# Optimization experiments

Hardware: AMD Instinct MI355X
Metric: run time of the kernel (lower is better)

The kernel has to match this reference:

```python
import jax, jax.numpy as jnp
import numpy as np

N_USER, N_ENTITY, N_RELATION = 100000, 2000000, 64
BATCH, N_NEIGHBOR, DIM = 65536, 8, 16
L2_WEIGHT = 1e-4


def setup_inputs() -> dict:
    key = jax.random.key(0)
    ks = jax.random.split(key, 10)
    inp = {
        # parameters: torch.rand(..)*2-1 -> uniform(-1,1)
        "user_emb": jax.random.uniform(ks[0], (N_USER, DIM), jnp.float32, -1.0, 1.0),
        "entity_emb": jax.random.uniform(ks[1], (N_ENTITY, DIM), jnp.float32, -1.0, 1.0),
        "relation_emb": jax.random.uniform(ks[2], (N_RELATION, DIM), jnp.float32, -1.0, 1.0),
        "agg_W": jax.random.normal(ks[3], (DIM, DIM), jnp.float32) * (1.0 / np.sqrt(DIM)),
        "agg_b": jnp.zeros((DIM,), jnp.float32),
        "labels": jnp.round(jax.random.uniform(ks[4], (BATCH,), jnp.float32)),
        "user_indices": jax.random.randint(ks[5], (BATCH,), 0, N_USER, jnp.int32),
        "item_indices": jax.random.randint(ks[6], (BATCH,), 0, N_ENTITY, jnp.int32),
        "adj_entity": jax.random.randint(ks[7], (N_ENTITY, N_NEIGHBOR), 0, N_ENTITY, jnp.int32),
        "adj_relation": jax.random.randint(ks[8], (N_ENTITY, N_NEIGHBOR), 0, N_RELATION, jnp.int32),
    }
    return inp


def reference(user_emb, entity_emb, relation_emb, agg_W, agg_b, labels,
              user_indices, item_indices, adj_entity, adj_relation):
    # --- gathers (1-hop, n_iter=1) ---
    u = user_emb[user_indices]                      # [B, D]
    self_vec = entity_emb[item_indices]             # [B, D]
    nbr_e = adj_entity[item_indices]                # [B, K]
    nbr_r = adj_relation[item_indices]              # [B, K]
    nbr_vecs = entity_emb[nbr_e]                    # [B, K, D]
    rel_vecs = relation_emb[nbr_r]                  # [B, K, D]

    # --- SumAggregator: user-relation attention over neighbors ---
    scores = jnp.mean(u[:, None, :] * rel_vecs, axis=-1)     # [B, K]
    attn = jax.nn.softmax(scores, axis=-1)                   # [B, K]
    nbr_agg = jnp.einsum('bk,bkd->bd', attn, nbr_vecs)       # [B, D]

    # Linear(dim,dim) + tanh (act on last hop)
    item_emb = jnp.tanh((self_vec + nbr_agg) @ agg_W.T + agg_b)  # [B, D]

    # --- score + BCE loss + L2 ---
    logits = jnp.sum(u * item_emb, axis=1)                   # [B]
    # -y*log(sigmoid(x)) - (1-y)*log(1-sigmoid(x)), stable form
    base_loss = jnp.mean(-labels * jax.nn.log_sigmoid(logits)
                         - (1.0 - labels) * jax.nn.log_sigmoid(-logits))
    l2 = 0.5 * (jnp.sum(user_emb ** 2) + jnp.sum(entity_emb ** 2)
                + jnp.sum(relation_emb ** 2))
    return base_loss + L2_WEIGHT * l2
```

## Files before the change

### kernel.cpp

```cpp
#include <hip/hip_runtime.h>
#include <math.h>

#define BATCH     65536
#define NNBR      8
#define DIM       16
#define HALF_L2W  5.0e-5f

#define BLOCK     256
#define GRID      2048
#define N_SBLK    1024
#define STH       (N_SBLK * BLOCK)
#define ROWS_PB   64

#define N_E4      8000000
#define N_U4      400000
#define N_R4      256

#define E_ITERS   (N_E4 / STH)
#define E_TAIL    (N_E4 - E_ITERS * STH)
#define U_TAIL    (N_U4 - STH)

__device__ __forceinline__ float sq4(float4 v) {
    return v.x * v.x + v.y * v.y + v.z * v.z + v.w * v.w;
}

__global__ void __launch_bounds__(BLOCK, 4)
fused_kernel(const float4* __restrict__ ue4,
             const float4* __restrict__ ee4,
             const float4* __restrict__ re4,
             const float*  __restrict__ W,
             const float4* __restrict__ b4,
             const float*  __restrict__ labels,
             const int*    __restrict__ uidx,
             const int*    __restrict__ iidx,
             const int4*   __restrict__ adjE4,
             const int4*   __restrict__ adjR4,
             float* __restrict__ ws) {
    float l2 = 0.0f, bce = 0.0f;

    const int role = blockIdx.x & 1;
    const int rid  = blockIdx.x >> 1;

    if (role == 0) {
        const int tid = rid * BLOCK + threadIdx.x;
        const float4* p = ee4 + tid;
        #pragma unroll
        for (int k = 0; k < E_ITERS; ++k) l2 += sq4(p[k * STH]);
        if (tid < E_TAIL) l2 += sq4(p[E_ITERS * STH]);
        l2 += sq4(ue4[tid]);
        if (tid < U_TAIL) l2 += sq4(ue4[tid + STH]);
        if (tid < N_R4)   l2 += sq4(re4[tid]);
    } else {
        __shared__ float sWT[DIM * DIM];
        __shared__ float4 sb4[DIM / 4];
        if (threadIdx.x < DIM * DIM)
            sWT[threadIdx.x] = W[(threadIdx.x & 15) * DIM + (threadIdx.x >> 4)];
        if (threadIdx.x < DIM / 4) sb4[threadIdx.x] = b4[threadIdx.x];
        __syncthreads();

        const int lane4 = threadIdx.x & 3;
        const int rgrp  = threadIdx.x >> 2;
        const int row   = rid * ROWS_PB + rgrp;

        const int ui = uidx[row];
        const int it = iidx[row];
        const float4 u4  = ue4[ui * 4 + lane4];
        const float4 sv4 = ee4[it * 4 + lane4];
        const int4 a0 = adjE4[it * 2], a1 = adjE4[it * 2 + 1];
        const int4 r0 = adjR4[it * 2], r1 = adjR4[it * 2 + 1];

        const int ne[NNBR] = {a0.x, a0.y, a0.z, a0.w, a1.x, a1.y, a1.z, a1.w};
        const int nr[NNBR] = {r0.x, r0.y, r0.z, r0.w, r1.x, r1.y, r1.z, r1.w};

        float4 nv[NNBR];
        float sc[NNBR];
        #pragma unroll
        for (int k = 0; k < NNBR; ++k) {
            const float4 rv = re4[nr[k] * 4 + lane4];
            nv[k] = ee4[ne[k] * 4 + lane4];
            float s = u4.x * rv.x + u4.y * rv.y + u4.z * rv.z + u4.w * rv.w;
            s += __shfl_xor(s, 1, 4);
            s += __shfl_xor(s, 2, 4);
            sc[k] = s * (1.0f / 16.0f);
        }

        float m = sc[0];
        #pragma unroll
        for (int k = 1; k < NNBR; ++k) m = fmaxf(m, sc[k]);
        float e[NNBR], den = 0.0f;
        #pragma unroll
        for (int k = 0; k < NNBR; ++k) { e[k] = __expf(sc[k] - m); den += e[k]; }
        const float inv = 1.0f / den;

        float4 agg = make_float4(0.f, 0.f, 0.f, 0.f);
        #pragma unroll
        for (int k = 0; k < NNBR; ++k) {
            agg.x += e[k] * nv[k].x; agg.y += e[k] * nv[k].y;
            agg.z += e[k] * nv[k].z; agg.w += e[k] * nv[k].w;
        }

        float4 x4;
        x4.x = sv4.x + agg.x * inv; x4.y = sv4.y + agg.y * inv;
        x4.z = sv4.z + agg.z * inv; x4.w = sv4.w + agg.w * inv;

        float xall[DIM];
        #pragma unroll
        for (int src = 0; src < 4; ++src) {
            xall[4 * src + 0] = __shfl(x4.x, src, 4);
            xall[4 * src + 1] = __shfl(x4.y, src, 4);
            xall[4 * src + 2] = __shfl(x4.z, src, 4);
            xall[4 * src + 3] = __shfl(x4.w, src, 4);
        }

        const float4* sWT4 = (const float4*)sWT;
        float4 acc = sb4[lane4];
        #pragma unroll
        for (int j = 0; j < DIM; ++j) {
            const float4 wv = sWT4[j * 4 + lane4];
            acc.x += xall[j] * wv.x; acc.y += xall[j] * wv.y;
            acc.z += xall[j] * wv.z; acc.w += xall[j] * wv.w;
        }
        float4 item;
        item.x = tanhf(acc.x); item.y = tanhf(acc.y);
        item.z = tanhf(acc.z); item.w = tanhf(acc.w);

        float lg = u4.x * item.x + u4.y * item.y + u4.z * item.z + u4.w * item.w;
        lg += __shfl_xor(lg, 1, 4);
        lg += __shfl_xor(lg, 2, 4);

        if (lane4 == 0) {
            const float y = labels[row];
            bce = fmaxf(lg, 0.0f) - lg * y + log1pf(__expf(-fabsf(lg)));
        }
    }

    #pragma unroll
    for (int o = 32; o > 0; o >>= 1) {
        bce += __shfl_down(bce, o);
        l2  += __shfl_down(l2, o);
    }
    __shared__ float sred[8];
    const int wid = threadIdx.x >> 6;
    if ((threadIdx.x & 63) == 0) { sred[wid] = l2; sred[4 + wid] = bce; }
    __syncthreads();
    if (threadIdx.x == 0) {
        ws[2 * blockIdx.x]     = sred[0] + sred[1] + sred[2] + sred[3];
        ws[2 * blockIdx.x + 1] = sred[4] + sred[5] + sred[6] + sred[7];
    }
}

__global__ void __launch_bounds__(256)
finalize_kernel(const float* __restrict__ ws, float* __restrict__ out) {
    float l2 = 0.0f, bce = 0.0f;
    #pragma unroll
    for (int k = 0; k < GRID / 256; ++k) {
        const int i = threadIdx.x + k * 256;
        l2  += ws[2 * i];
        bce += ws[2 * i + 1];
    }
    #pragma unroll
    for (int o = 32; o > 0; o >>= 1) {
        l2  += __shfl_down(l2, o);
        bce += __shfl_down(bce, o);
    }
    __shared__ float sred[8];
    const int wid = threadIdx.x >> 6;
    if ((threadIdx.x & 63) == 0) { sred[wid] = l2; sred[4 + wid] = bce; }
    __syncthreads();
    if (threadIdx.x == 0) {
        const float l2t  = sred[0] + sred[1] + sred[2] + sred[3];
        const float bcet = sred[4] + sred[5] + sred[6] + sred[7];
        out[0] = bcet * (1.0f / (float)BATCH) + HALF_L2W * l2t;
    }
}

extern "C" void kernel_launch(void* const* d_in, const int* in_sizes, int n_in,
                              void* d_out, int out_size, void* d_ws, size_t ws_size,
                              hipStream_t stream) {
    const float* user_emb     = (const float*)d_in[0];
    const float* entity_emb   = (const float*)d_in[1];
    const float* relation_emb = (const float*)d_in[2];
    const float* agg_W        = (const float*)d_in[3];
    const float* agg_b        = (const float*)d_in[4];
    const float* labels       = (const float*)d_in[5];
    const int*   user_indices = (const int*)d_in[6];
    const int*   item_indices = (const int*)d_in[7];
    const int*   adj_entity   = (const int*)d_in[8];
    const int*   adj_relation = (const int*)d_in[9];

    float* ws  = (float*)d_ws;
    float* out = (float*)d_out;

    fused_kernel<<<GRID, BLOCK, 0, stream>>>(
        (const float4*)user_emb, (const float4*)entity_emb, (const float4*)relation_emb,
        agg_W, (const float4*)agg_b, labels,
        user_indices, item_indices,
        (const int4*)adj_entity, (const int4*)adj_relation, ws);

    finalize_kernel<<<1, 256, 0, stream>>>(ws, out);
}
```

Before: 42.87 us.

## Split fused role-interleaved kernel into separate L2 streaming and row kernels

Replaces the single kernel that alternated L2-reduction blocks and per-row gather blocks with two kernels launched back to back: a 2048-block streaming L2 sum and a 1024-block row/BCE kernel. The streaming kernel now uses twice as many threads, so each thread handles fewer entity chunks. Separating the roles removes the role branch and lets each kernel get its own register and occupancy profile. The cost is an extra kernel launch, and the two phases no longer overlap within one grid.

Result: slower. 47.13 us (+9.9%).

```diff
diff --git a/kernel.cpp b/kernel.cpp
--- a/kernel.cpp
+++ b/kernel.cpp
@@ -6,158 +6,165 @@
 #define DIM       16
 #define HALF_L2W  5.0e-5f
 
-#define BLOCK     256
-#define GRID      2048
-#define N_SBLK    1024
-#define STH       (N_SBLK * BLOCK)
-#define ROWS_PB   64
-
+#define SBLOCK    256
+#define SGRID     2048
+#define STH       (SGRID * SBLOCK)
 #define N_E4      8000000
 #define N_U4      400000
 #define N_R4      256
-
 #define E_ITERS   (N_E4 / STH)
 #define E_TAIL    (N_E4 - E_ITERS * STH)
-#define U_TAIL    (N_U4 - STH)
+
+#define RBLOCK    256
+#define RGRID     1024
+#define ROWS_PB   64
+
+#define WS_BCE_OFF SGRID
 
 __device__ __forceinline__ float sq4(float4 v) {
     return v.x * v.x + v.y * v.y + v.z * v.z + v.w * v.w;
 }
 
-__global__ void __launch_bounds__(BLOCK, 4)
-fused_kernel(const float4* __restrict__ ue4,
-             const float4* __restrict__ ee4,
-             const float4* __restrict__ re4,
-             const float*  __restrict__ W,
-             const float4* __restrict__ b4,
-             const float*  __restrict__ labels,
-             const int*    __restrict__ uidx,
-             const int*    __restrict__ iidx,
-             const int4*   __restrict__ adjE4,
-             const int4*   __restrict__ adjR4,
-             float* __restrict__ ws) {
-    float l2 = 0.0f, bce = 0.0f;
-
-    const int role = blockIdx.x & 1;
-    const int rid  = blockIdx.x >> 1;
-
-    if (role == 0) {
-        const int tid = rid * BLOCK + threadIdx.x;
-        const float4* p = ee4 + tid;
-        #pragma unroll
-        for (int k = 0; k < E_ITERS; ++k) l2 += sq4(p[k * STH]);
-        if (tid < E_TAIL) l2 += sq4(p[E_ITERS * STH]);
-        l2 += sq4(ue4[tid]);
-        if (tid < U_TAIL) l2 += sq4(ue4[tid + STH]);
-        if (tid < N_R4)   l2 += sq4(re4[tid]);
-    } else {
-        __shared__ float sWT[DIM * DIM];
-        __shared__ float4 sb4[DIM / 4];
-        if (threadIdx.x < DIM * DIM)
-            sWT[threadIdx.x] = W[(threadIdx.x & 15) * DIM + (threadIdx.x >> 4)];
-        if (threadIdx.x < DIM / 4) sb4[threadIdx.x] = b4[threadIdx.x];
-        __syncthreads();
-
-        const int lane4 = threadIdx.x & 3;
-        const int rgrp  = threadIdx.x >> 2;
-        const int row   = rid * ROWS_PB + rgrp;
-
-        const int ui = uidx[row];
-        const int it = iidx[row];
-        const float4 u4  = ue4[ui * 4 + lane4];
-        const float4 sv4 = ee4[it * 4 + lane4];
-        const int4 a0 = adjE4[it * 2], a1 = adjE4[it * 2 + 1];
-        const int4 r0 = adjR4[it * 2], r1 = adjR4[it * 2 + 1];
-
-        const int ne[NNBR] = {a0.x, a0.y, a0.z, a0.w, a1.x, a1.y, a1.z, a1.w};
-        const int nr[NNBR] = {r0.x, r0.y, r0.z, r0.w, r1.x, r1.y, r1.z, r1.w};
-
-        float4 nv[NNBR];
-        float sc[NNBR];
-        #pragma unroll
-        for (int k = 0; k < NNBR; ++k) {
-            const float4 rv = re4[nr[k] * 4 + lane4];
-            nv[k] = ee4[ne[k] * 4 + lane4];
-            float s = u4.x * rv.x + u4.y * rv.y + u4.z * rv.z + u4.w * rv.w;
-            s += __shfl_xor(s, 1, 4);
-            s += __shfl_xor(s, 2, 4);
-            sc[k] = s * (1.0f / 16.0f);
-        }
-
-        float m = sc[0];
-        #pragma unroll
-        for (int k = 1; k < NNBR; ++k) m = fmaxf(m, sc[k]);
-        float e[NNBR], den = 0.0f;
-        #pragma unroll
-        for (int k = 0; k < NNBR; ++k) { e[k] = __expf(sc[k] - m); den += e[k]; }
-        const float inv = 1.0f / den;
-
-        float4 agg = make_float4(0.f, 0.f, 0.f, 0.f);
-        #pragma unroll
-        for (int k = 0; k < NNBR; ++k) {
-            agg.x += e[k] * nv[k].x; agg.y += e[k] * nv[k].y;
-            agg.z += e[k] * nv[k].z; agg.w += e[k] * nv[k].w;
-        }
-
-        float4 x4;
-        x4.x = sv4.x + agg.x * inv; x4.y = sv4.y + agg.y * inv;
-        x4.z = sv4.z + agg.z * inv; x4.w = sv4.w + agg.w * inv;
-
-        float xall[DIM];
-        #pragma unroll
-        for (int src = 0; src < 4; ++src) {
-            xall[4 * src + 0] = __shfl(x4.x, src, 4);
-            xall[4 * src + 1] = __shfl(x4.y, src, 4);
-            xall[4 * src + 2] = __shfl(x4.z, src, 4);
-            xall[4 * src + 3] = __shfl(x4.w, src, 4);
-        }
-
-        const float4* sWT4 = (const float4*)sWT;
-        float4 acc = sb4[lane4];
-        #pragma unroll
-        for (int j = 0; j < DIM; ++j) {
-            const float4 wv = sWT4[j * 4 + lane4];
-            acc.x += xall[j] * wv.x; acc.y += xall[j] * wv.y;
-            acc.z += xall[j] * wv.z; acc.w += xall[j] * wv.w;
-        }
-        float4 item;
-        item.x = tanhf(acc.x); item.y = tanhf(acc.y);
-        item.z = tanhf(acc.z); item.w = tanhf(acc.w);
-
-        float lg = u4.x * item.x + u4.y * item.y + u4.z * item.z + u4.w * item.w;
-        lg += __shfl_xor(lg, 1, 4);
-        lg += __shfl_xor(lg, 2, 4);
-
-        if (lane4 == 0) {
-            const float y = labels[row];
-            bce = fmaxf(lg, 0.0f) - lg * y + log1pf(__expf(-fabsf(lg)));
-        }
-    }
-
-    #pragma unroll
-    for (int o = 32; o > 0; o >>= 1) {
-        bce += __shfl_down(bce, o);
-        l2  += __shfl_down(l2, o);
-    }
-    __shared__ float sred[8];
+__global__ void __launch_bounds__(SBLOCK)
+stream_l2(const float4* __restrict__ ue4,
+          const float4* __restrict__ ee4,
+          const float4* __restrict__ re4,
+          float* __restrict__ ws) {
+    const int tid = blockIdx.x * SBLOCK + threadIdx.x;
+
+    float l2 = 0.0f;
+    const float4* p = ee4 + tid;
+    #pragma unroll
+    for (int k = 0; k < E_ITERS; ++k) l2 += sq4(p[k * STH]);
+    if (tid < E_TAIL) l2 += sq4(p[E_ITERS * STH]);
+    if (tid < N_U4)   l2 += sq4(ue4[tid]);
+    if (tid < N_R4)   l2 += sq4(re4[tid]);
+
+    #pragma unroll
+    for (int o = 32; o > 0; o >>= 1) l2 += __shfl_down(l2, o);
+
+    __shared__ float sred[4];
     const int wid = threadIdx.x >> 6;
-    if ((threadIdx.x & 63) == 0) { sred[wid] = l2; sred[4 + wid] = bce; }
-    __syncthreads();
-    if (threadIdx.x == 0) {
-        ws[2 * blockIdx.x]     = sred[0] + sred[1] + sred[2] + sred[3];
-        ws[2 * blockIdx.x + 1] = sred[4] + sred[5] + sred[6] + sred[7];
-    }
+    if ((threadIdx.x & 63) == 0) sred[wid] = l2;
+    __syncthreads();
+    if (threadIdx.x == 0)
+        ws[blockIdx.x] = sred[0] + sred[1] + sred[2] + sred[3];
+}
+
+__global__ void __launch_bounds__(RBLOCK)
+row_kernel(const float4* __restrict__ ue4,
+           const float4* __restrict__ ee4,
+           const float4* __restrict__ re4,
+           const float*  __restrict__ W,
+           const float4* __restrict__ b4,
+           const float*  __restrict__ labels,
+           const int*    __restrict__ uidx,
+           const int*    __restrict__ iidx,
+           const int4*   __restrict__ adjE4,
+           const int4*   __restrict__ adjR4,
+           float* __restrict__ ws) {
+    __shared__ float sWT[DIM * DIM];
+    __shared__ float4 sbias[DIM / 4];
+    sWT[threadIdx.x] = W[(threadIdx.x & 15) * DIM + (threadIdx.x >> 4)];
+    if (threadIdx.x < DIM / 4) sbias[threadIdx.x] = b4[threadIdx.x];
+    __syncthreads();
+
+    const int lane4 = threadIdx.x & 3;
+    const int row   = blockIdx.x * ROWS_PB + (threadIdx.x >> 2);
+
+    const int ui = uidx[row];
+    const int it = iidx[row];
+    const float4 u4  = ue4[ui * 4 + lane4];
+    const float4 sv4 = ee4[it * 4 + lane4];
+    const int4 a0 = adjE4[it * 2], a1 = adjE4[it * 2 + 1];
+    const int4 r0 = adjR4[it * 2], r1 = adjR4[it * 2 + 1];
+
+    const int ne[NNBR] = {a0.x, a0.y, a0.z, a0.w, a1.x, a1.y, a1.z, a1.w};
+    const int nr[NNBR] = {r0.x, r0.y, r0.z, r0.w, r1.x, r1.y, r1.z, r1.w};
+
+    float4 nv[NNBR];
+    float sc[NNBR];
+    #pragma unroll
+    for (int k = 0; k < NNBR; ++k) {
+        const float4 rv = re4[nr[k] * 4 + lane4];
+        nv[k] = ee4[ne[k] * 4 + lane4];
+        float s = u4.x * rv.x + u4.y * rv.y + u4.z * rv.z + u4.w * rv.w;
+        s += __shfl_xor(s, 1, 4);
+        s += __shfl_xor(s, 2, 4);
+        sc[k] = s * (1.0f / 16.0f);
+    }
+
+    float m = sc[0];
+    #pragma unroll
+    for (int k = 1; k < NNBR; ++k) m = fmaxf(m, sc[k]);
+    float e[NNBR], den = 0.0f;
+    #pragma unroll
+    for (int k = 0; k < NNBR; ++k) { e[k] = __expf(sc[k] - m); den += e[k]; }
+    const float inv = 1.0f / den;
+
+    float4 agg = make_float4(0.f, 0.f, 0.f, 0.f);
+    #pragma unroll
+    for (int k = 0; k < NNBR; ++k) {
+        agg.x += e[k] * nv[k].x; agg.y += e[k] * nv[k].y;
+        agg.z += e[k] * nv[k].z; agg.w += e[k] * nv[k].w;
+    }
+
+    float4 x4;
+    x4.x = sv4.x + agg.x * inv; x4.y = sv4.y + agg.y * inv;
+    x4.z = sv4.z + agg.z * inv; x4.w = sv4.w + agg.w * inv;
+
+    float xall[DIM];
+    #pragma unroll
+    for (int src = 0; src < 4; ++src) {
+        xall[4 * src + 0] = __shfl(x4.x, src, 4);
+        xall[4 * src + 1] = __shfl(x4.y, src, 4);
+        xall[4 * src + 2] = __shfl(x4.z, src, 4);
+        xall[4 * src + 3] = __shfl(x4.w, src, 4);
+    }
+
+    const float4* sWT4 = (const float4*)sWT;
+    float4 acc = sbias[lane4];
+    #pragma unroll
+    for (int j = 0; j < DIM; ++j) {
+        const float4 wv = sWT4[j * 4 + lane4];
+        acc.x += xall[j] * wv.x; acc.y += xall[j] * wv.y;
+        acc.z += xall[j] * wv.z; acc.w += xall[j] * wv.w;
+    }
+    float4 item;
+    item.x = tanhf(acc.x); item.y = tanhf(acc.y);
+    item.z = tanhf(acc.z); item.w = tanhf(acc.w);
+
+    float lg = u4.x * item.x + u4.y * item.y + u4.z * item.z + u4.w * item.w;
+    lg += __shfl_xor(lg, 1, 4);
+    lg += __shfl_xor(lg, 2, 4);
+
+    float bce = 0.0f;
+    if (lane4 == 0) {
+        const float y = labels[row];
+        bce = fmaxf(lg, 0.0f) - lg * y + log1pf(__expf(-fabsf(lg)));
+    }
+
+    #pragma unroll
+    for (int o = 32; o > 0; o >>= 1) bce += __shfl_down(bce, o);
+
+    __shared__ float sred[4];
+    const int wid = threadIdx.x >> 6;
+    if ((threadIdx.x & 63) == 0) sred[wid] = bce;
+    __syncthreads();
+    if (threadIdx.x == 0)
+        ws[WS_BCE_OFF + blockIdx.x] = sred[0] + sred[1] + sred[2] + sred[3];
 }
 
 __global__ void __launch_bounds__(256)
 finalize_kernel(const float* __restrict__ ws, float* __restrict__ out) {
     float l2 = 0.0f, bce = 0.0f;
     #pragma unroll
-    for (int k = 0; k < GRID / 256; ++k) {
-        const int i = threadIdx.x + k * 256;
-        l2  += ws[2 * i];
-        bce += ws[2 * i + 1];
-    }
+    for (int k = 0; k < SGRID / 256; ++k)
+        l2 += ws[threadIdx.x + k * 256];
+    #pragma unroll
+    for (int k = 0; k < RGRID / 256; ++k)
+        bce += ws[WS_BCE_OFF + threadIdx.x + k * 256];
+
     #pragma unroll
     for (int o = 32; o > 0; o >>= 1) {
         l2  += __shfl_down(l2, o);
@@ -177,25 +184,24 @@
 extern "C" void kernel_launch(void* const* d_in, const int* in_sizes, int n_in,
                               void* d_out, int out_size, void* d_ws, size_t ws_size,
                               hipStream_t stream) {
-    const float* user_emb     = (const float*)d_in[0];
-    const float* entity_emb   = (const float*)d_in[1];
-    const float* relation_emb = (const float*)d_in[2];
-    const float* agg_W        = (const float*)d_in[3];
-    const float* agg_b        = (const float*)d_in[4];
-    const float* labels       = (const float*)d_in[5];
-    const int*   user_indices = (const int*)d_in[6];
-    const int*   item_indices = (const int*)d_in[7];
-    const int*   adj_entity   = (const int*)d_in[8];
-    const int*   adj_relation = (const int*)d_in[9];
+    const float4* ue4    = (const float4*)d_in[0];
+    const float4* ee4    = (const float4*)d_in[1];
+    const float4* re4    = (const float4*)d_in[2];
+    const float*  W      = (const float*)d_in[3];
+    const float4* b4     = (const float4*)d_in[4];
+    const float*  labels = (const float*)d_in[5];
+    const int*    uidx   = (const int*)d_in[6];
+    const int*    iidx   = (const int*)d_in[7];
+    const int4*   adjE4  = (const int4*)d_in[8];
+    const int4*   adjR4  = (const int4*)d_in[9];
 
     float* ws  = (float*)d_ws;
     float* out = (float*)d_out;
 
-    fused_kernel<<<GRID, BLOCK, 0, stream>>>(
-        (const float4*)user_emb, (const float4*)entity_emb, (const float4*)relation_emb,
-        agg_W, (const float4*)agg_b, labels,
-        user_indices, item_indices,
-        (const int4*)adj_entity, (const int4*)adj_relation, ws);
+    stream_l2<<<SGRID, SBLOCK, 0, stream>>>(ue4, ee4, re4, ws);
+
+    row_kernel<<<RGRID, RBLOCK, 0, stream>>>(
+        ue4, ee4, re4, W, b4, labels, uidx, iidx, adjE4, adjR4, ws);
 
     finalize_kernel<<<1, 256, 0, stream>>>(ws, out);
 }
```
